# Performance work log

Hardware: AMD Instinct MI355X
Metric: run time of the kernel (lower is better)

The kernel has to match this reference:

```python
import jax, jax.numpy as jnp
import numpy as np

ALPHA = 0.9  # init alpha, adj='DAD'


def setup_inputs() -> dict:
    key = jax.random.key(0)
    k1, k2, k3, k4 = jax.random.split(key, 4)
    N, C, E = 100000, 64, 3200000
    labels = jax.random.uniform(k1, (N, C), dtype=jnp.float32)
    mask = jax.random.randint(k2, (N,), 0, 2).astype(bool)
    src = jax.random.randint(k3, (E,), 0, N, dtype=jnp.int64)
    dst = jax.random.randint(k4, (E,), 0, N, dtype=jnp.int64)
    return {"labels": labels, "mask": mask, "src": src, "dst": dst, "num_layers": 10}


def reference(labels, mask, src, dst, num_layers):
    N = labels.shape[0]
    # mask: y = zeros; y[mask] = labels[mask]
    y0 = jnp.where(mask[:, None], labels, jnp.zeros((), labels.dtype))
    last = (1.0 - ALPHA) * y0  # confidence = 1
    # in-degrees via scatter-count at dst, clamped to >= 1
    degs = jax.ops.segment_sum(jnp.ones(dst.shape, labels.dtype), dst, num_segments=N)
    degs = jnp.maximum(degs, 1.0)
    norm = (degs ** -0.5)[:, None]  # DAD: D^-1/2 on both sides

    def step(y, _):
        y = norm * y                                   # left D^-1/2
        h = jax.ops.segment_sum(y[src], dst, num_segments=N)  # A @ y (copy_u + sum)
        y = ALPHA * h * norm                           # right D^-1/2
        y = jnp.clip(last + y, 0.0, 1.0)               # post_step clamp
        return y, None

    y, _ = jax.lax.scan(step, y0, None, length=num_layers)
    return y
```

## Files before the change

### kernel.cpp

```cpp
#include <hip/hip_runtime.h>
#include <hip/hip_fp16.h>


#define ALPHA 0.9f
#define C 64
#define BSHIFT 9
#define NCHUNK 256


__global__ void chunk_hist_kernel(const int* __restrict__ dst, int* __restrict__ cnt,
                                  int E, int epc) {
    __shared__ int h[256];
    h[threadIdx.x] = 0;
    __syncthreads();
    int c = blockIdx.x;
    int e1 = min(c * epc + epc, E);
    for (int e = c * epc + threadIdx.x; e < e1; e += 256) {
        int d = __builtin_nontemporal_load(&dst[e]);
        atomicAdd(&h[d >> BSHIFT], 1);
    }
    __syncthreads();
    cnt[c * 256 + threadIdx.x] = h[threadIdx.x];
}

__global__ void bucket_scan_kernel(int* __restrict__ cnt, int* __restrict__ bucket_base,
                                   int* __restrict__ row_ptr, int N, int E) {
    __shared__ int tmp[256];
    int b = threadIdx.x;
    int s = 0;
    for (int c = 0; c < NCHUNK; ++c) {
        int t = cnt[c * 256 + b];
        cnt[c * 256 + b] = s;
        s += t;
    }
    tmp[b] = s;
    __syncthreads();
    int v = s;
    for (int off = 1; off < 256; off <<= 1) {
        int add = (b >= off) ? tmp[b - off] : 0;
        __syncthreads();
        tmp[b] += add;
        __syncthreads();
    }
    bucket_base[b] = tmp[b] - v;
    if (b == 255) { bucket_base[256] = tmp[255]; row_ptr[N] = E; }
}

__global__ void bucket_scatter_kernel(const int* __restrict__ src, const int* __restrict__ dst,
                                      const int* __restrict__ cnt,
                                      const int* __restrict__ bucket_base,
                                      unsigned* __restrict__ tmp, int E, int epc) {
    __shared__ int cur[256];
    int c = blockIdx.x;
    cur[threadIdx.x] = bucket_base[threadIdx.x] + cnt[c * 256 + threadIdx.x];
    __syncthreads();
    int e1 = min(c * epc + epc, E);
    for (int e = c * epc + threadIdx.x; e < e1; e += 256) {
        int d = __builtin_nontemporal_load(&dst[e]);
        int s = __builtin_nontemporal_load(&src[e]);
        int pos = atomicAdd(&cur[d >> BSHIFT], 1);
        tmp[pos] = ((unsigned)(d & 511) << 23) | (unsigned)s;
    }
}

__global__ void bucket_sort_kernel(const unsigned* __restrict__ tmp,
                                   const int* __restrict__ bucket_base,
                                   int* __restrict__ row_ptr,
                                   float* __restrict__ norm,
                                   int* __restrict__ col, int N) {
    __shared__ int ldeg[512];
    __shared__ int lexc[512];
    __shared__ int lcur[512];
    __shared__ int stmp[256];
    int b = blockIdx.x;
    int lo = b << BSHIFT;
    int nn = min(512, N - lo);
    int ebeg = bucket_base[b];
    int eend = bucket_base[b + 1];
    int t = threadIdx.x;
    ldeg[t] = 0; ldeg[t + 256] = 0;
    __syncthreads();
    for (int e = ebeg + t; e < eend; e += 256) {
        atomicAdd(&ldeg[tmp[e] >> 23], 1);
    }
    __syncthreads();
    int d0 = ldeg[2 * t], d1 = ldeg[2 * t + 1];
    int p = d0 + d1;
    stmp[t] = p;
    __syncthreads();
    for (int off = 1; off < 256; off <<= 1) {
        int add = (t >= off) ? stmp[t - off] : 0;
        __syncthreads();
        stmp[t] += add;
        __syncthreads();
    }
    int excp = stmp[t] - p;
    lexc[2 * t] = excp;
    lexc[2 * t + 1] = excp + d0;
    __syncthreads();
    for (int i = t; i < nn; i += 256) {
        int rp = ebeg + lexc[i];
        row_ptr[lo + i] = rp;
        lcur[i] = rp;
        norm[lo + i] = rsqrtf(fmaxf((float)ldeg[i], 1.0f));
    }
    __syncthreads();
    for (int e = ebeg + t; e < eend; e += 256) {
        unsigned pk = tmp[e];
        int pos = atomicAdd(&lcur[pk >> 23], 1);
        col[pos] = (int)(pk & 0x7FFFFFu);
    }
}


__global__ void init_z_kernel(const float* __restrict__ labels,
                              const int* __restrict__ mask,
                              const float* __restrict__ norm,
                              __half* __restrict__ z,
                              __half* __restrict__ last16,
                              int total8 ) {
    int i = blockIdx.x * blockDim.x + threadIdx.x;
    if (i >= total8) return;
    int row = i >> 3;
    float4 a = ((const float4*)labels)[i * 2];
    float4 b = ((const float4*)labels)[i * 2 + 1];
    bool mk = mask[row] != 0;
    float m = mk ? norm[row] : 0.0f;
    __half2 h[4];
    h[0] = __floats2half2_rn(m * a.x, m * a.y);
    h[1] = __floats2half2_rn(m * a.z, m * a.w);
    h[2] = __floats2half2_rn(m * b.x, m * b.y);
    h[3] = __floats2half2_rn(m * b.z, m * b.w);
    ((float4*)z)[i] = *(const float4*)h;
    if (last16) {
        float ml = mk ? (1.0f - ALPHA) : 0.0f;
        __half2 g[4];
        g[0] = __floats2half2_rn(ml * a.x, ml * a.y);
        g[1] = __floats2half2_rn(ml * a.z, ml * a.w);
        g[2] = __floats2half2_rn(ml * b.x, ml * b.y);
        g[3] = __floats2half2_rn(ml * b.z, ml * b.w);
        ((float4*)last16)[i] = *(const float4*)g;
    }
}

template <bool OUT_FP32>
__global__ void prop_kernel(const __half* __restrict__ z_old,
                            void* __restrict__ z_new_v,
                            const int* __restrict__ row_ptr,
                            const int* __restrict__ col,
                            const float* __restrict__ norm,
                            const __half* __restrict__ last16,
                            const float* __restrict__ labels,
                            const int* __restrict__ mask, int N) {
    int gtid = blockIdx.x * blockDim.x + threadIdx.x;
    int wid = gtid >> 6;
    int lane = threadIdx.x & 63;
    int node = (wid << 1) + (lane >> 5);
    int sub = (lane >> 3) & 3;
    int ch8 = lane & 7;

    bool ok = node < N;
    int beg = 0, end = 0;
    if (ok) { beg = row_ptr[node]; end = row_ptr[node + 1]; }
    int deg = end - beg;
    int lastc = max(end - 1, 0);
    int Tl = (deg + 3) >> 2;
    int T = max(Tl, __shfl_xor(Tl, 32, 64));

    float acc[8];
#pragma unroll
    for (int k = 0; k < 8; ++k) acc[k] = 0.0f;

    if (T > 0) {
        int base = beg + sub;

        float n0, n1, n2, n3, n4, n5, n6, n7;
        float4 r0, r1, r2, r3, r4, r5, r6, r7;

#define FETCH(t, nv, rv)                                                      \
        do {                                                                  \
            int pp = base + ((t) << 2);                                       \
            int pcl = min(pp, lastc);                                         \
            int sv = col[pcl];                                                \
            nv = (pp < end) ? 1.0f : 0.0f;                                    \
            rv = ((const float4*)(z_old + (size_t)sv * C))[ch8];              \
        } while (0)

#define CONSUME(nv, rv)                                                       \
        do {                                                                  \
            const __half* hh = (const __half*)&rv;                            \
            acc[0] = fmaf(__half2float(hh[0]), nv, acc[0]);                   \
            acc[1] = fmaf(__half2float(hh[1]), nv, acc[1]);                   \
            acc[2] = fmaf(__half2float(hh[2]), nv, acc[2]);                   \
            acc[3] = fmaf(__half2float(hh[3]), nv, acc[3]);                   \
            acc[4] = fmaf(__half2float(hh[4]), nv, acc[4]);                   \
            acc[5] = fmaf(__half2float(hh[5]), nv, acc[5]);                   \
            acc[6] = fmaf(__half2float(hh[6]), nv, acc[6]);                   \
            acc[7] = fmaf(__half2float(hh[7]), nv, acc[7]);                   \
        } while (0)

        FETCH(0, n0, r0); FETCH(1, n1, r1); FETCH(2, n2, r2); FETCH(3, n3, r3);
        FETCH(4, n4, r4); FETCH(5, n5, r5); FETCH(6, n6, r6); FETCH(7, n7, r7);
        int t = 8;
        for (; t + 8 <= T; t += 8) {
            CONSUME(n0, r0); FETCH(t + 0, n0, r0);
            CONSUME(n1, r1); FETCH(t + 1, n1, r1);
            CONSUME(n2, r2); FETCH(t + 2, n2, r2);
            CONSUME(n3, r3); FETCH(t + 3, n3, r3);
            CONSUME(n4, r4); FETCH(t + 4, n4, r4);
            CONSUME(n5, r5); FETCH(t + 5, n5, r5);
            CONSUME(n6, r6); FETCH(t + 6, n6, r6);
            CONSUME(n7, r7); FETCH(t + 7, n7, r7);
        }
        int rr = T - t;
        if (rr > 0) { CONSUME(n0, r0); FETCH(t + 0, n0, r0); }
        if (rr > 1) { CONSUME(n1, r1); FETCH(t + 1, n1, r1); }
        if (rr > 2) { CONSUME(n2, r2); FETCH(t + 2, n2, r2); }
        if (rr > 3) { CONSUME(n3, r3); FETCH(t + 3, n3, r3); }
        if (rr > 4) { CONSUME(n4, r4); FETCH(t + 4, n4, r4); }
        if (rr > 5) { CONSUME(n5, r5); FETCH(t + 5, n5, r5); }
        if (rr > 6) { CONSUME(n6, r6); FETCH(t + 6, n6, r6); }
        CONSUME(n0, r0); CONSUME(n1, r1); CONSUME(n2, r2); CONSUME(n3, r3);
        CONSUME(n4, r4); CONSUME(n5, r5); CONSUME(n6, r6); CONSUME(n7, r7);
#undef FETCH
#undef CONSUME
    }

#pragma unroll
    for (int k = 0; k < 8; ++k) {
        acc[k] += __shfl_xor(acc[k], 8, 64);
        acc[k] += __shfl_xor(acc[k], 16, 64);
    }

    if (sub == 0 && ok) {
        float nr = norm[node];
        float anr = ALPHA * nr;
        float la[8];
        if (last16) {
            float4 lv = ((const float4*)(last16 + (size_t)node * C))[ch8];
            const __half* lh = (const __half*)&lv;
#pragma unroll
            for (int k = 0; k < 8; ++k) la[k] = __half2float(lh[k]);
        } else {
            const float* lrow = labels + (size_t)node * C + ch8 * 8;
            float4 A = ((const float4*)lrow)[0];
            float4 Bv = ((const float4*)lrow)[1];
            float m = (mask[node] != 0) ? (1.0f - ALPHA) : 0.0f;
            la[0] = m * A.x;  la[1] = m * A.y;  la[2] = m * A.z;  la[3] = m * A.w;
            la[4] = m * Bv.x; la[5] = m * Bv.y; la[6] = m * Bv.z; la[7] = m * Bv.w;
        }
        float o[8];
#pragma unroll
        for (int k = 0; k < 8; ++k)
            o[k] = fminf(fmaxf(la[k] + anr * acc[k], 0.0f), 1.0f);
        if (OUT_FP32) {
            float* orow = (float*)z_new_v + (size_t)node * C + ch8 * 8;
            float4 v0; v0.x = o[0]; v0.y = o[1]; v0.z = o[2]; v0.w = o[3];
            float4 v1; v1.x = o[4]; v1.y = o[5]; v1.z = o[6]; v1.w = o[7];
            ((float4*)orow)[0] = v0;
            ((float4*)orow)[1] = v1;
        } else {
            __half2 h[4];
            h[0] = __floats2half2_rn(nr * o[0], nr * o[1]);
            h[1] = __floats2half2_rn(nr * o[2], nr * o[3]);
            h[2] = __floats2half2_rn(nr * o[4], nr * o[5]);
            h[3] = __floats2half2_rn(nr * o[6], nr * o[7]);
            __half* orow = (__half*)z_new_v + (size_t)node * C + ch8 * 8;
            *(float4*)orow = *(const float4*)h;
        }
    }
}


__global__ void zero_f32_kernel(float* __restrict__ p, int n) {
    int i = blockIdx.x * blockDim.x + threadIdx.x;
    if (i < n) p[i] = 0.0f;
}
__global__ void deg_count_f_kernel(const int* __restrict__ dst, float* __restrict__ deg, int E) {
    int i = blockIdx.x * blockDim.x + threadIdx.x;
    if (i < E) atomicAdd(&deg[dst[i]], 1.0f);
}
__global__ void make_norm_f_kernel(float* __restrict__ deg, int N) {
    int i = blockIdx.x * blockDim.x + threadIdx.x;
    if (i < N) deg[i] = rsqrtf(fmaxf(deg[i], 1.0f));
}
__global__ void init_yh_kernel(const float* __restrict__ labels, const int* __restrict__ mask,
                               float* __restrict__ y, float* __restrict__ h, int total4) {
    int i = blockIdx.x * blockDim.x + threadIdx.x;
    if (i >= total4) return;
    int row = i >> 4;
    float4 lv = ((const float4*)labels)[i];
    float m = (mask[row] != 0) ? 1.0f : 0.0f;
    float4 yv; yv.x = m * lv.x; yv.y = m * lv.y; yv.z = m * lv.z; yv.w = m * lv.w;
    ((float4*)y)[i] = yv;
    float4 z; z.x = 0.f; z.y = 0.f; z.z = 0.f; z.w = 0.f;
    ((float4*)h)[i] = z;
}
__global__ void scatter_kernel(const float* __restrict__ y, const int* __restrict__ src,
                               const int* __restrict__ dst, const float* __restrict__ norm,
                               float* __restrict__ h, int E) {
    int gtid = blockIdx.x * blockDim.x + threadIdx.x;
    int e = gtid >> 6;
    int lane = threadIdx.x & 63;
    if (e >= E) return;
    int s = src[e]; int d = dst[e];
    float v = y[(size_t)s * C + lane] * norm[s];
    atomicAdd(&h[(size_t)d * C + lane], v);
}
__global__ void finalize_kernel(const float* __restrict__ labels, const int* __restrict__ mask,
                                const float* __restrict__ norm, float* __restrict__ h,
                                float* __restrict__ y, int total4) {
    int i = blockIdx.x * blockDim.x + threadIdx.x;
    if (i >= total4) return;
    int row = i >> 4;
    float4 hv = ((float4*)h)[i];
    float4 lv = ((const float4*)labels)[i];
    float m = (mask[row] != 0) ? (1.0f - ALPHA) : 0.0f;
    float nr = norm[row];
    float4 o;
    o.x = fminf(fmaxf(m * lv.x + ALPHA * hv.x * nr, 0.0f), 1.0f);
    o.y = fminf(fmaxf(m * lv.y + ALPHA * hv.y * nr, 0.0f), 1.0f);
    o.z = fminf(fmaxf(m * lv.z + ALPHA * hv.z * nr, 0.0f), 1.0f);
    o.w = fminf(fmaxf(m * lv.w + ALPHA * hv.w * nr, 0.0f), 1.0f);
    ((float4*)y)[i] = o;
    float4 z; z.x = 0.f; z.y = 0.f; z.z = 0.f; z.w = 0.f;
    ((float4*)h)[i] = z;
}


extern "C" void kernel_launch(void* const* d_in, const int* in_sizes, int n_in,
                              void* d_out, int out_size, void* d_ws, size_t ws_size,
                              hipStream_t stream) {
    const float* labels = (const float*)d_in[0];
    const int*   mask   = (const int*)d_in[1];
    const int*   src    = (const int*)d_in[2];
    const int*   dst    = (const int*)d_in[3];

    const int N = in_sizes[1];
    const int E = in_sizes[2];
    const int num_layers = 10;
    const int B = 256;

    size_t fixed_ints = (size_t)257 + (size_t)NCHUNK * 256 + (N + 1) + N + E;
    size_t ybytes = (size_t)N * C * 2;
    size_t tmpbytes = (size_t)E * 4;
    size_t span = (tmpbytes > ybytes ? tmpbytes : ybytes);
    size_t need_base = fixed_ints * 4 + 256 + ybytes + span;
    size_t need_l16  = need_base + ybytes;
    bool pack_ok = (N < (1 << 23));

    if (ws_size >= need_base && pack_ok) {
        char* w = (char*)d_ws;
        int*   bucket_base = (int*)w;             w += 257 * 4;
        int*   cnt         = (int*)w;             w += (size_t)NCHUNK * 256 * 4;
        int*   row_ptr     = (int*)w;             w += (size_t)(N + 1) * 4;
        float* norm        = (float*)w;           w += (size_t)N * 4;
        int*   col         = (int*)w;             w += (size_t)E * 4;
        w = (char*)(((uintptr_t)w + 255) & ~(uintptr_t)255);
        __half* zA         = (__half*)w;          w += ybytes;
        __half* zB         = (__half*)w;
        unsigned* tmp      = (unsigned*)zB;
        __half* last16     = (ws_size >= need_l16) ? (__half*)(w + span) : nullptr;

        int epc = (E + NCHUNK - 1) / NCHUNK;
        int NB = (N + 511) >> BSHIFT;

        chunk_hist_kernel<<<NCHUNK, 256, 0, stream>>>(dst, cnt, E, epc);
        bucket_scan_kernel<<<1, 256, 0, stream>>>(cnt, bucket_base, row_ptr, N, E);
        bucket_scatter_kernel<<<NCHUNK, 256, 0, stream>>>(src, dst, cnt, bucket_base,
                                                          tmp, E, epc);
        bucket_sort_kernel<<<NB, 256, 0, stream>>>(tmp, bucket_base, row_ptr,
                                                   norm, col, N);

        int total8 = N * C / 8;
        init_z_kernel<<<(total8 + B - 1) / B, B, 0, stream>>>(labels, mask, norm,
                                                              zA, last16, total8);
        const int nwaves = (N + 1) >> 1;
        const int prop_blocks = (int)(((size_t)nwaves * 64 + B - 1) / B);
        for (int l = 0; l < num_layers - 1; ++l) {
            __half* zi = (l & 1) ? zB : zA;
            __half* zo = (l & 1) ? zA : zB;
            prop_kernel<false><<<prop_blocks, B, 0, stream>>>(zi, zo, row_ptr, col,
                                                              norm, last16,
                                                              labels, mask, N);
        }
        prop_kernel<true><<<prop_blocks, B, 0, stream>>>(zB, d_out, row_ptr, col,
                                                         norm, last16,
                                                         labels, mask, N);
    } else {
        const int total4 = N * C / 4;
        float* y = (float*)d_out;
        float* wsf = (float*)d_ws;
        float* norm = wsf;
        float* h = wsf + ((N + 15) & ~15);
        zero_f32_kernel<<<(N + B - 1) / B, B, 0, stream>>>(norm, N);
        deg_count_f_kernel<<<(E + B - 1) / B, B, 0, stream>>>(dst, norm, E);
        make_norm_f_kernel<<<(N + B - 1) / B, B, 0, stream>>>(norm, N);
        init_yh_kernel<<<(total4 + B - 1) / B, B, 0, stream>>>(labels, mask, y, h, total4);
        const int scatter_blocks = (int)(((size_t)E * C + B - 1) / B);
        for (int l = 0; l < num_layers; ++l) {
            scatter_kernel<<<scatter_blocks, B, 0, stream>>>(y, src, dst, norm, h, E);
            finalize_kernel<<<(total4 + B - 1) / B, B, 0, stream>>>(labels, mask, norm,
                                                                    h, y, total4);
        }
    }
}
```

Baseline: 751.3 us.

## Store propagated node features as uint8 with per-row scale instead of fp16

The intermediate label matrix between propagation layers is now quantized to 8-bit unsigned integers with one float scale per node, replacing fp16 storage. The scale folds in the degree normalization, so the gather loop multiplies dequantized bytes by the neighbour's scale. This halves the bytes gathered per neighbour row and shrinks the working set so more of it can stay in cache. In exchange it adds per-row max reductions via shuffles, an extra scale load per edge, and coarser quantization error that compounds over the layers.

```diff
diff --git a/kernel.cpp b/kernel.cpp
--- a/kernel.cpp
+++ b/kernel.cpp
@@ -6,6 +6,9 @@
 #define C 64
 #define BSHIFT 9
 #define NCHUNK 256
+
+typedef float f32x4 __attribute__((ext_vector_type(4)));
+typedef unsigned int u32;
 
 
 __global__ void chunk_hist_kernel(const int* __restrict__ dst, int* __restrict__ cnt,
@@ -113,39 +116,57 @@
 }
 
 
-__global__ void init_z_kernel(const float* __restrict__ labels,
-                              const int* __restrict__ mask,
-                              const float* __restrict__ norm,
-                              __half* __restrict__ z,
-                              __half* __restrict__ last16,
-                              int total8 ) {
+__global__ void init_z8_kernel(const float* __restrict__ labels,
+                               const int* __restrict__ mask,
+                               const float* __restrict__ norm,
+                               unsigned char* __restrict__ z8,
+                               float* __restrict__ scale,
+                               __half* __restrict__ last16,
+                               int total8 ) {
     int i = blockIdx.x * blockDim.x + threadIdx.x;
     if (i >= total8) return;
-    int row = i >> 3;
-    float4 a = ((const float4*)labels)[i * 2];
-    float4 b = ((const float4*)labels)[i * 2 + 1];
-    bool mk = mask[row] != 0;
-    float m = mk ? norm[row] : 0.0f;
-    __half2 h[4];
-    h[0] = __floats2half2_rn(m * a.x, m * a.y);
-    h[1] = __floats2half2_rn(m * a.z, m * a.w);
-    h[2] = __floats2half2_rn(m * b.x, m * b.y);
-    h[3] = __floats2half2_rn(m * b.z, m * b.w);
-    ((float4*)z)[i] = *(const float4*)h;
+    int node = i >> 3;
+    int g = i & 7;
+    const float* lrow = labels + (size_t)node * C + g * 8;
+    f32x4 a  = __builtin_nontemporal_load((const f32x4*)lrow);
+    f32x4 bv = __builtin_nontemporal_load((const f32x4*)lrow + 1);
+    bool mk = mask[node] != 0;
+    float v[8] = {a.x, a.y, a.z, a.w, bv.x, bv.y, bv.z, bv.w};
+    float lm = 0.0f;
+    if (mk) {
+#pragma unroll
+        for (int k = 0; k < 8; ++k) lm = fmaxf(lm, v[k]);
+    }
+    lm = fmaxf(lm, __shfl_xor(lm, 1, 64));
+    lm = fmaxf(lm, __shfl_xor(lm, 2, 64));
+    lm = fmaxf(lm, __shfl_xor(lm, 4, 64));
+    float inv = (mk && lm > 0.0f) ? 255.0f / lm : 0.0f;
+    u32 q0 = 0, q1 = 0;
+#pragma unroll
+    for (int k = 0; k < 4; ++k) q0 |= ((u32)(v[k] * inv + 0.5f)) << (8 * k);
+#pragma unroll
+    for (int k = 0; k < 4; ++k) q1 |= ((u32)(v[k + 4] * inv + 0.5f)) << (8 * k);
+    uint2 qq; qq.x = q0; qq.y = q1;
+    ((uint2*)(z8 + (size_t)node * C))[g] = qq;
+    if (g == 0) scale[node] = mk ? norm[node] * lm * (1.0f / 255.0f) : 0.0f;
     if (last16) {
         float ml = mk ? (1.0f - ALPHA) : 0.0f;
-        __half2 g[4];
-        g[0] = __floats2half2_rn(ml * a.x, ml * a.y);
-        g[1] = __floats2half2_rn(ml * a.z, ml * a.w);
-        g[2] = __floats2half2_rn(ml * b.x, ml * b.y);
-        g[3] = __floats2half2_rn(ml * b.z, ml * b.w);
-        ((float4*)last16)[i] = *(const float4*)g;
-    }
-}
+        __half2 h[4];
+        h[0] = __floats2half2_rn(ml * v[0], ml * v[1]);
+        h[1] = __floats2half2_rn(ml * v[2], ml * v[3]);
+        h[2] = __floats2half2_rn(ml * v[4], ml * v[5]);
+        h[3] = __floats2half2_rn(ml * v[6], ml * v[7]);
+        ((float4*)(last16 + (size_t)node * C))[g] = *(const float4*)h;
+    }
+}
+
 
 template <bool OUT_FP32>
-__global__ void prop_kernel(const __half* __restrict__ z_old,
-                            void* __restrict__ z_new_v,
+__global__ void prop_kernel(const unsigned char* __restrict__ z8_old,
+                            const float* __restrict__ scale_old,
+                            unsigned char* __restrict__ z8_new,
+                            float* __restrict__ scale_new,
+                            void* __restrict__ out_f32,
                             const int* __restrict__ row_ptr,
                             const int* __restrict__ col,
                             const float* __restrict__ norm,
@@ -175,28 +196,29 @@
         int base = beg + sub;
 
         float n0, n1, n2, n3, n4, n5, n6, n7;
-        float4 r0, r1, r2, r3, r4, r5, r6, r7;
+        uint2 r0, r1, r2, r3, r4, r5, r6, r7;
 
 #define FETCH(t, nv, rv)                                                      \
         do {                                                                  \
             int pp = base + ((t) << 2);                                       \
             int pcl = min(pp, lastc);                                         \
             int sv = col[pcl];                                                \
-            nv = (pp < end) ? 1.0f : 0.0f;                                    \
-            rv = ((const float4*)(z_old + (size_t)sv * C))[ch8];              \
+            float sc = scale_old[sv];                                         \
+            nv = (pp < end) ? sc : 0.0f;                                      \
+            rv = ((const uint2*)(z8_old + (size_t)sv * C))[ch8];              \
         } while (0)
 
 #define CONSUME(nv, rv)                                                       \
         do {                                                                  \
-            const __half* hh = (const __half*)&rv;                            \
-            acc[0] = fmaf(__half2float(hh[0]), nv, acc[0]);                   \
-            acc[1] = fmaf(__half2float(hh[1]), nv, acc[1]);                   \
-            acc[2] = fmaf(__half2float(hh[2]), nv, acc[2]);                   \
-            acc[3] = fmaf(__half2float(hh[3]), nv, acc[3]);                   \
-            acc[4] = fmaf(__half2float(hh[4]), nv, acc[4]);                   \
-            acc[5] = fmaf(__half2float(hh[5]), nv, acc[5]);                   \
-            acc[6] = fmaf(__half2float(hh[6]), nv, acc[6]);                   \
-            acc[7] = fmaf(__half2float(hh[7]), nv, acc[7]);                   \
+            u32 q0 = rv.x, q1 = rv.y;                                         \
+            acc[0] = fmaf((float)(q0 & 0xffu),         nv, acc[0]);           \
+            acc[1] = fmaf((float)((q0 >> 8) & 0xffu),  nv, acc[1]);           \
+            acc[2] = fmaf((float)((q0 >> 16) & 0xffu), nv, acc[2]);           \
+            acc[3] = fmaf((float)(q0 >> 24),           nv, acc[3]);           \
+            acc[4] = fmaf((float)(q1 & 0xffu),         nv, acc[4]);           \
+            acc[5] = fmaf((float)((q1 >> 8) & 0xffu),  nv, acc[5]);           \
+            acc[6] = fmaf((float)((q1 >> 16) & 0xffu), nv, acc[6]);           \
+            acc[7] = fmaf((float)(q1 >> 24),           nv, acc[7]);           \
         } while (0)
 
         FETCH(0, n0, r0); FETCH(1, n1, r1); FETCH(2, n2, r2); FETCH(3, n3, r3);
@@ -254,19 +276,27 @@
         for (int k = 0; k < 8; ++k)
             o[k] = fminf(fmaxf(la[k] + anr * acc[k], 0.0f), 1.0f);
         if (OUT_FP32) {
-            float* orow = (float*)z_new_v + (size_t)node * C + ch8 * 8;
+            float* orow = (float*)out_f32 + (size_t)node * C + ch8 * 8;
             float4 v0; v0.x = o[0]; v0.y = o[1]; v0.z = o[2]; v0.w = o[3];
             float4 v1; v1.x = o[4]; v1.y = o[5]; v1.z = o[6]; v1.w = o[7];
             ((float4*)orow)[0] = v0;
             ((float4*)orow)[1] = v1;
         } else {
-            __half2 h[4];
-            h[0] = __floats2half2_rn(nr * o[0], nr * o[1]);
-            h[1] = __floats2half2_rn(nr * o[2], nr * o[3]);
-            h[2] = __floats2half2_rn(nr * o[4], nr * o[5]);
-            h[3] = __floats2half2_rn(nr * o[6], nr * o[7]);
-            __half* orow = (__half*)z_new_v + (size_t)node * C + ch8 * 8;
-            *(float4*)orow = *(const float4*)h;
+            float m = o[0];
+#pragma unroll
+            for (int k = 1; k < 8; ++k) m = fmaxf(m, o[k]);
+            m = fmaxf(m, __shfl_xor(m, 1, 64));
+            m = fmaxf(m, __shfl_xor(m, 2, 64));
+            m = fmaxf(m, __shfl_xor(m, 4, 64));
+            float inv = (m > 0.0f) ? 255.0f / m : 0.0f;
+            u32 q0 = 0, q1 = 0;
+#pragma unroll
+            for (int k = 0; k < 4; ++k) q0 |= ((u32)(o[k] * inv + 0.5f)) << (8 * k);
+#pragma unroll
+            for (int k = 0; k < 4; ++k) q1 |= ((u32)(o[k + 4] * inv + 0.5f)) << (8 * k);
+            uint2 qq; qq.x = q0; qq.y = q1;
+            ((uint2*)(z8_new + (size_t)node * C))[ch8] = qq;
+            if (ch8 == 0) scale_new[node] = m * nr * (1.0f / 255.0f);
         }
     }
 }
@@ -342,11 +372,13 @@
     const int B = 256;
 
     size_t fixed_ints = (size_t)257 + (size_t)NCHUNK * 256 + (N + 1) + N + E;
-    size_t ybytes = (size_t)N * C * 2;
+    size_t z8bytes = (size_t)N * C;
     size_t tmpbytes = (size_t)E * 4;
-    size_t span = (tmpbytes > ybytes ? tmpbytes : ybytes);
-    size_t need_base = fixed_ints * 4 + 256 + ybytes + span;
-    size_t need_l16  = need_base + ybytes;
+    size_t span = (tmpbytes > 2 * z8bytes ? tmpbytes : 2 * z8bytes);
+    size_t scbytes = (size_t)N * 4;
+    size_t l16bytes = (size_t)N * C * 2;
+    size_t need_base = fixed_ints * 4 + 256 + span + 2 * scbytes;
+    size_t need_l16  = need_base + l16bytes;
     bool pack_ok = (N < (1 << 23));
 
     if (ws_size >= need_base && pack_ok) {
@@ -357,10 +389,13 @@
         float* norm        = (float*)w;           w += (size_t)N * 4;
         int*   col         = (int*)w;             w += (size_t)E * 4;
         w = (char*)(((uintptr_t)w + 255) & ~(uintptr_t)255);
-        __half* zA         = (__half*)w;          w += ybytes;
-        __half* zB         = (__half*)w;
-        unsigned* tmp      = (unsigned*)zB;
-        __half* last16     = (ws_size >= need_l16) ? (__half*)(w + span) : nullptr;
+        unsigned char* z8A = (unsigned char*)w;
+        unsigned char* z8B = z8A + z8bytes;
+        unsigned* tmp      = (unsigned*)z8A;
+        w += span;
+        float* scA         = (float*)w;           w += scbytes;
+        float* scB         = (float*)w;           w += scbytes;
+        __half* last16     = (ws_size >= need_l16) ? (__half*)w : nullptr;
 
         int epc = (E + NCHUNK - 1) / NCHUNK;
         int NB = (N + 511) >> BSHIFT;
@@ -372,21 +407,24 @@
         bucket_sort_kernel<<<NB, 256, 0, stream>>>(tmp, bucket_base, row_ptr,
                                                    norm, col, N);
 
-        int total8 = N * C / 8;
-        init_z_kernel<<<(total8 + B - 1) / B, B, 0, stream>>>(labels, mask, norm,
-                                                              zA, last16, total8);
+        int total8 = N * 8;
+        init_z8_kernel<<<(total8 + B - 1) / B, B, 0, stream>>>(labels, mask, norm,
+                                                               z8A, scA, last16,
+                                                               total8);
         const int nwaves = (N + 1) >> 1;
         const int prop_blocks = (int)(((size_t)nwaves * 64 + B - 1) / B);
         for (int l = 0; l < num_layers - 1; ++l) {
-            __half* zi = (l & 1) ? zB : zA;
-            __half* zo = (l & 1) ? zA : zB;
-            prop_kernel<false><<<prop_blocks, B, 0, stream>>>(zi, zo, row_ptr, col,
-                                                              norm, last16,
-                                                              labels, mask, N);
+            unsigned char* zi = (l & 1) ? z8B : z8A;
+            unsigned char* zo = (l & 1) ? z8A : z8B;
+            float* si = (l & 1) ? scB : scA;
+            float* so = (l & 1) ? scA : scB;
+            prop_kernel<false><<<prop_blocks, B, 0, stream>>>(zi, si, zo, so, nullptr,
+                                                              row_ptr, col, norm,
+                                                              last16, labels, mask, N);
         }
-        prop_kernel<true><<<prop_blocks, B, 0, stream>>>(zB, d_out, row_ptr, col,
-                                                         norm, last16,
-                                                         labels, mask, N);
+        prop_kernel<true><<<prop_blocks, B, 0, stream>>>(z8B, scB, nullptr, nullptr,
+                                                         d_out, row_ptr, col, norm,
+                                                         last16, labels, mask, N);
     } else {
         const int total4 = N * C / 4;
         float* y = (float*)d_out;
```

Result: slower. 818.8 us (+9.0%).
